# Performance work log

Hardware: AMD Instinct MI355X
Metric: run time of the kernel (lower is better)

## Reference

```python
import jax
import jax.numpy as jnp
from jax import lax
import numpy as np

DIM = 64
HIDDEN = int(DIM * 2.66)      # 170
C2 = HIDDEN * 2               # 340
PATCH = 8


def setup_inputs() -> dict:
    key = jax.random.key(0)
    k1, k2, k3, k4, k5 = jax.random.split(key, 5)
    B, H, W = 4, 256, 256
    x = jax.random.normal(k1, (B, DIM, H, W), dtype=jnp.float32)
    # project_in: 1x1 conv, stored as [out, in]
    w_in = jax.random.normal(k2, (C2, DIM), dtype=jnp.float32) * (1.0 / np.sqrt(DIM))
    # depthwise 3x3 conv weight [C2, 1, 3, 3]
    w_dw = jax.random.normal(k3, (C2, 1, 3, 3), dtype=jnp.float32) * (1.0 / 3.0)
    # learned rFFT filter, init ones in torch; perturb for a nontrivial test
    fft_w = 1.0 + 0.1 * jax.random.normal(k4, (C2, 1, 1, PATCH, PATCH // 2 + 1), dtype=jnp.float32)
    # project_out: 1x1 conv [out, in]
    w_out = jax.random.normal(k5, (DIM, HIDDEN), dtype=jnp.float32) * (1.0 / np.sqrt(HIDDEN))
    return {"x": x, "w_in": w_in, "w_dw": w_dw, "fft_w": fft_w, "w_out": w_out}


def reference(x, w_in, w_dw, fft_w, w_out):
    p = PATCH
    # project_in (1x1 conv)
    x = jnp.einsum('bchw,oc->bohw', x, w_in)
    B, C, H, W = x.shape
    # patchify: b c (h p1) (w p2) -> b c h w p1 p2
    xp = x.reshape(B, C, H // p, p, W // p, p).transpose(0, 1, 2, 4, 3, 5)
    # per-patch rFFT2, elementwise learned filter, inverse
    xf = jnp.fft.rfft2(xp)                       # [B,C,h,w,8,5] complex
    xf = xf * fft_w                              # fft_w broadcasts [C,1,1,8,5]
    xp = jnp.fft.irfft2(xf, s=(p, p))
    # unpatchify
    x = xp.transpose(0, 1, 2, 4, 3, 5).reshape(B, C, H, W)
    # depthwise 3x3 conv, padding 1
    x = lax.conv_general_dilated(
        x, w_dw, window_strides=(1, 1), padding=((1, 1), (1, 1)),
        dimension_numbers=('NCHW', 'OIHW', 'NCHW'), feature_group_count=C)
    # GELU gate
    x1, x2 = jnp.split(x, 2, axis=1)
    x = jax.nn.gelu(x1, approximate=False) * x2
    # project_out (1x1 conv)
    return jnp.einsum('bchw,oc->bohw', x, w_out)
```

## Files before the change

kernel.cpp:

```cpp
#include <hip/hip_runtime.h>
#include <hip/hip_bf16.h>

#define C2 340
#define HID 170
#define NB 4
#define HGT 256
#define WID 256
#define HW (HGT*WID)
#define BAND 128

typedef unsigned short u16;
typedef unsigned int u32;
typedef float f32x4 __attribute__((ext_vector_type(4)));
typedef short s16x8 __attribute__((ext_vector_type(8)));

__device__ __forceinline__ float bf2f(u16 u) {
  union { u32 i; float f; } v; v.i = ((u32)u) << 16; return v.f;
}
__device__ __forceinline__ u16 f2bf(float f) {
  union { float f; u32 i; } v; v.f = f;
  u32 x = v.i;
  return (u16)((x + 0x7fffu + ((x >> 16) & 1u)) >> 16);
}

__device__ __forceinline__ float gelu(float v) {
  const float u = v * 0.70710678118654752f;
  const float ax = fabsf(u);
  const float t = __builtin_amdgcn_rcpf(__builtin_fmaf(0.3275911f, ax, 1.f));
  float p = __builtin_fmaf(1.061405429f, t, -1.453152027f);
  p = __builtin_fmaf(p, t, 1.421413741f);
  p = __builtin_fmaf(p, t, -0.284496736f);
  p = __builtin_fmaf(p, t, 0.254829592f);
  const float e = __builtin_amdgcn_exp2f(-1.4426950408889634f * ax * ax);
  float er = 1.f - p * t * e;
  er = copysignf(er, u);
  return 0.5f * v * (1.f + er);
}

__device__ const float COSTAB[8] = {1.f, 0.70710678118654752f, 0.f, -0.70710678118654752f,
                                    -1.f, -0.70710678118654752f, 0.f, 0.70710678118654752f};

__global__ __launch_bounds__(256) void k_prep(const float* __restrict__ w_in,
                                              const float* __restrict__ w_out,
                                              const float* __restrict__ fw,
                                              u16* __restrict__ wf,
                                              u16* __restrict__ wof,
                                              u16* __restrict__ mf) {
  __shared__ float kern[64];
  const int blk = blockIdx.x;
  if (blk < C2) {
    const int c = blk;
    if (threadIdx.x < 64) {
      const int a = threadIdx.x >> 3, bb = threadIdx.x & 7;
      float acc = 0.f;
      for (int u = 0; u < 8; ++u)
        for (int v = 0; v < 8; ++v) {
          const float wv = (v <= 4) ? fw[c*40 + u*5 + v]
                                    : fw[c*40 + ((8-u)&7)*5 + (8-v)];
          acc += wv * COSTAB[(u*a + v*bb) & 7];
        }
      kern[threadIdx.x] = acc * (1.f/64.f);
    }
    __syncthreads();
    #pragma unroll
    for (int q = 0; q < 16; ++q) {
      const int e = q * 256 + threadIdx.x;
      const int r = e & 7;
      const int l = (e >> 3) & 63;
      const int sb = e >> 9;
      const int s = sb & 1, nblk = sb >> 1;
      const int k = s*32 + ((l >> 4) << 3) + r;
      const int a = k >> 3, bcol = k & 7;
      const int n = nblk*16 + (l & 15);
      const int i = n >> 3, j = n & 7;
      mf[(size_t)c * 4096 + e] = f2bf(kern[(((i - a) & 7) << 3) + ((j - bcol) & 7)]);
    }
  } else if (blk == C2) {
    for (int e = threadIdx.x; e < 22*2*64*8; e += 256) {
      const int r = e & 7;
      const int l = (e >> 3) & 63;
      const int ts = e >> 9;
      const int s = ts & 1, t = ts >> 1;
      const int m = t*16 + (l & 15);
      const int k = s*32 + ((l >> 4) << 3) + r;
      wf[e] = (m < C2) ? f2bf(w_in[m*64 + k]) : (u16)0;
    }
  } else {
    for (int e = threadIdx.x; e < 4*6*64*8; e += 256) {
      const int r = e & 7;
      const int l = (e >> 3) & 63;
      const int mk = e >> 9;
      const int kc = mk % 6, mt = mk / 6;
      const int m = mt*16 + (l & 15);
      const int k = kc*32 + ((l >> 4) << 3) + r;
      wof[e] = (k < HID) ? f2bf(w_out[m*HID + k]) : (u16)0;
    }
  }
}

__global__ __launch_bounds__(256) void k_projin2(const float* __restrict__ x,
                                                 const u16* __restrict__ wf,
                                                 u16* __restrict__ mid) {
  __shared__ __align__(16) u16 st[16][264];
  const int b = blockIdx.x >> 8;
  const int pix_blk = (blockIdx.x & 255) << 8;
  const int w = threadIdx.x >> 6;
  const int lane = threadIdx.x & 63;
  const int lm = lane & 15, lh = lane >> 4;
  const int pix0 = pix_blk + w*64;

  s16x8 Bf[4][2];
  {
    const float* xp = x + (size_t)b * 64 * HW + pix0;
    #pragma unroll
    for (int g = 0; g < 4; ++g)
      #pragma unroll
      for (int s = 0; s < 2; ++s) {
        s16x8 t;
        #pragma unroll
        for (int r = 0; r < 8; ++r) {
          const int ch = s*32 + lh*8 + r;
          t[r] = (short)f2bf(xp[(size_t)ch * HW + g*16 + lm]);
        }
        Bf[g][s] = t;
      }
  }
  u16* mp = mid + (size_t)b * C2 * HW + pix_blk;
  const int ch_rd = threadIdx.x >> 4;
  const int seg = threadIdx.x & 15;
  for (int t = 0; t < 22; ++t) {
    const s16x8 A0 = *(const s16x8*)(wf + ((t*2 + 0)*64 + lane)*8);
    const s16x8 A1 = *(const s16x8*)(wf + ((t*2 + 1)*64 + lane)*8);
    f32x4 ac[4];
    #pragma unroll
    for (int g = 0; g < 4; ++g) {
      ac[g] = (f32x4){0.f,0.f,0.f,0.f};
      ac[g] = __builtin_amdgcn_mfma_f32_16x16x32_bf16(A0, Bf[g][0], ac[g], 0,0,0);
      ac[g] = __builtin_amdgcn_mfma_f32_16x16x32_bf16(A1, Bf[g][1], ac[g], 0,0,0);
    }
    __syncthreads();
    #pragma unroll
    for (int g = 0; g < 4; ++g)
      #pragma unroll
      for (int r = 0; r < 4; ++r)
        st[lh*4 + r][w*64 + g*16 + lm] = f2bf(ac[g][r]);
    __syncthreads();
    const int ch = t*16 + ch_rd;
    if (ch < C2) {
      u16* dst = mp + (size_t)ch * HW + seg*16;
      *(uint4*)dst       = *(const uint4*)&st[ch_rd][seg*16];
      *(uint4*)(dst + 8) = *(const uint4*)&st[ch_rd][seg*16 + 8];
    }
  }
}

__global__ __launch_bounds__(512) void k_pcgate(const u16* __restrict__ mid,
                                                const u16* __restrict__ mf,
                                                const float* __restrict__ w_dw,
                                                u16* __restrict__ gbuf, int hb) {
  __shared__ __align__(16) u16 st[2][18][272];
  const int c = blockIdx.x % HID;
  const int b = blockIdx.x / HID;
  const int P0 = hb >> 3;

  const int w = threadIdx.x >> 6;
  const int lane = threadIdx.x & 63;
  const int lm = lane & 15, lh = lane >> 4;
  const int ch2 = w >> 2;
  const int wl = w & 3;
  const int prow_sub = wl >> 1;
  const int phalf = wl & 1;
  const int ch = c + ch2*HID;
  const int colbase = (phalf*16 + lh*4)*8 + (lm & 7) + 8;

  for (int i = threadIdx.x; i < 2*18*34; i += 512)
    ((uint4*)st)[i] = make_uint4(0,0,0,0);

  s16x8 Bc[4][2];
  const u16* mfc = mf + (size_t)ch * 4096;
  #pragma unroll
  for (int nb = 0; nb < 4; ++nb)
    #pragma unroll
    for (int ks = 0; ks < 2; ++ks)
      Bc[nb][ks] = *(const s16x8*)(mfc + ((nb*2 + ks)*64 + lane)*8);
  const u16* chan = mid + (size_t)(b*C2 + ch) * HW;
  const float* wd1 = w_dw + c * 9;
  const float* wd2 = w_dw + (c + HID) * 9;
  __syncthreads();

  for (int it = 0; it < 8; ++it) {
    const int py2 = P0 + it*2 + 2;
    if (it == 0) {
      for (int i = threadIdx.x; i < 2*34; i += 512)
        ((uint4*)&st[i/34][0][0])[i%34] = make_uint4(0,0,0,0);
    } else {
      for (int i = threadIdx.x; i < 2*34; i += 512)
        ((uint4*)&st[i/34][0][0])[i%34] = ((const uint4*)&st[i/34][16][0])[i%34];
    }
    if (py2 >= 32) {
      for (int i = threadIdx.x; i < 2*34; i += 512)
        ((uint4*)&st[i/34][17][0])[i%34] = make_uint4(0,0,0,0);
    }
    __syncthreads();
    {
      const int py = P0 + it*2 + prow_sub;
      const u16* aptr = chan + (size_t)(py*8 + lh)*WID + (phalf*16 + lm)*8;
      const s16x8 A0 = *(const s16x8*)(aptr);
      const s16x8 A1 = *(const s16x8*)(aptr + 4*WID);
      const int rowb = 1 + prow_sub*8 + (lm >> 3);
      #pragma unroll
      for (int nb = 0; nb < 4; ++nb) {
        f32x4 acc = {0.f,0.f,0.f,0.f};
        acc = __builtin_amdgcn_mfma_f32_16x16x32_bf16(A0, Bc[nb][0], acc, 0,0,0);
        acc = __builtin_amdgcn_mfma_f32_16x16x32_bf16(A1, Bc[nb][1], acc, 0,0,0);
        #pragma unroll
        for (int r = 0; r < 4; ++r)
          st[ch2][rowb + nb*2][colbase + r*8] = f2bf(acc[r]);
      }
    }
    if (wl < 2) {
      if (py2 < 32) {
        const u16* ap = chan + (size_t)(py2*8 + lh)*WID + (phalf*16 + lm)*8;
        const s16x8 A0 = *(const s16x8*)(ap);
        const s16x8 A1 = *(const s16x8*)(ap + 4*WID);
        f32x4 acc = {0.f,0.f,0.f,0.f};
        acc = __builtin_amdgcn_mfma_f32_16x16x32_bf16(A0, Bc[0][0], acc, 0,0,0);
        acc = __builtin_amdgcn_mfma_f32_16x16x32_bf16(A1, Bc[0][1], acc, 0,0,0);
        if ((lm >> 3) == 0) {
          #pragma unroll
          for (int r = 0; r < 4; ++r)
            st[ch2][17][colbase + r*8] = f2bf(acc[r]);
        }
      }
    } else if (it == 0) {
      const int pym = P0 - 1;
      if (pym >= 0) {
        const u16* ap = chan + (size_t)(pym*8 + lh)*WID + (phalf*16 + lm)*8;
        const s16x8 A0 = *(const s16x8*)(ap);
        const s16x8 A1 = *(const s16x8*)(ap + 4*WID);
        f32x4 acc = {0.f,0.f,0.f,0.f};
        acc = __builtin_amdgcn_mfma_f32_16x16x32_bf16(A0, Bc[3][0], acc, 0,0,0);
        acc = __builtin_amdgcn_mfma_f32_16x16x32_bf16(A1, Bc[3][1], acc, 0,0,0);
        if ((lm >> 3) == 1) {
          #pragma unroll
          for (int r = 0; r < 4; ++r)
            st[ch2][0][colbase + r*8] = f2bf(acc[r]);
        }
      }
    }
    __syncthreads();
    {
      const int rg = threadIdx.x >> 5;
      const int px0 = (threadIdx.x & 31) * 8;
      float ax[8], ay[8];
      #pragma unroll
      for (int p = 0; p < 8; ++p) { ax[p] = 0.f; ay[p] = 0.f; }
      #pragma unroll
      for (int wr = 0; wr < 3; ++wr) {
        const u16* r1 = &st[0][rg + wr][px0];
        const u16* r2 = &st[1][rg + wr][px0];
        const s16x8 L1 = *(const s16x8*)r1, M1 = *(const s16x8*)(r1 + 8), R1 = *(const s16x8*)(r1 + 16);
        const s16x8 L2 = *(const s16x8*)r2, M2 = *(const s16x8*)(r2 + 8), R2 = *(const s16x8*)(r2 + 16);
        float cx[10], cy[10];
        cx[0] = bf2f((u16)L1[7]);  cy[0] = bf2f((u16)L2[7]);
        #pragma unroll
        for (int p = 0; p < 8; ++p) { cx[p+1] = bf2f((u16)M1[p]); cy[p+1] = bf2f((u16)M2[p]); }
        cx[9] = bf2f((u16)R1[0]);  cy[9] = bf2f((u16)R2[0]);
        const float w1a = wd1[wr*3+0], w1b = wd1[wr*3+1], w1c = wd1[wr*3+2];
        const float w2a = wd2[wr*3+0], w2b = wd2[wr*3+1], w2c = wd2[wr*3+2];
        #pragma unroll
        for (int p = 0; p < 8; ++p) {
          ax[p] += w1a*cx[p] + w1b*cx[p+1] + w1c*cx[p+2];
          ay[p] += w2a*cy[p] + w2b*cy[p+1] + w2c*cy[p+2];
        }
      }
      u32 pk[4];
      #pragma unroll
      for (int p2 = 0; p2 < 4; ++p2) {
        const float g0 = gelu(ax[2*p2])   * ay[2*p2];
        const float g1 = gelu(ax[2*p2+1]) * ay[2*p2+1];
        pk[p2] = (u32)f2bf(g0) | ((u32)f2bf(g1) << 16);
      }
      u16* gp = gbuf + (((size_t)(b*HID + c)) * BAND + (size_t)(it*16 + rg)) * WID + px0;
      *(uint4*)gp = make_uint4(pk[0], pk[1], pk[2], pk[3]);
    }
    __syncthreads();
  }
}

__global__ __launch_bounds__(256) void k_projout2(const u16* __restrict__ gbuf,
                                                  const u16* __restrict__ wof,
                                                  float* __restrict__ out, int hb) {
  const int b = blockIdx.x >> 7;
  const int p0 = (blockIdx.x & 127) << 8;
  const int w = threadIdx.x >> 6;
  const int lane = threadIdx.x & 63;
  const int lm = lane & 15, lh = lane >> 4;
  const size_t BW = (size_t)BAND * WID;
  const u16* gb = gbuf + (size_t)b * HID * BW + p0 + w*64 + lm;

  f32x4 acc[4][4];
  #pragma unroll
  for (int mt = 0; mt < 4; ++mt)
    #pragma unroll
    for (int ng = 0; ng < 4; ++ng)
      acc[mt][ng] = (f32x4){0.f,0.f,0.f,0.f};

  #pragma unroll
  for (int kc = 0; kc < 6; ++kc) {
    s16x8 A[4];
    #pragma unroll
    for (int mt = 0; mt < 4; ++mt)
      A[mt] = *(const s16x8*)(wof + ((mt*6 + kc)*64 + lane)*8);
    #pragma unroll
    for (int ng = 0; ng < 4; ++ng) {
      s16x8 Bf;
      #pragma unroll
      for (int r = 0; r < 8; ++r) {
        int c = kc*32 + lh*8 + r;
        if (kc == 5) c = min(c, HID - 1);
        Bf[r] = (short)gb[(size_t)c * BW + ng*16];
      }
      #pragma unroll
      for (int mt = 0; mt < 4; ++mt)
        acc[mt][ng] = __builtin_amdgcn_mfma_f32_16x16x32_bf16(A[mt], Bf, acc[mt][ng], 0,0,0);
    }
  }
  float* ob = out + (size_t)b * 64 * HW + (size_t)hb * WID + p0 + w*64 + lm;
  #pragma unroll
  for (int mt = 0; mt < 4; ++mt)
    #pragma unroll
    for (int ng = 0; ng < 4; ++ng)
      #pragma unroll
      for (int r = 0; r < 4; ++r)
        ob[(size_t)(mt*16 + lh*4 + r) * HW + ng*16] = acc[mt][ng][r];
}

extern "C" void kernel_launch(void* const* d_in, const int* in_sizes, int n_in,
                              void* d_out, int out_size, void* d_ws, size_t ws_size,
                              hipStream_t stream) {
  const float* x     = (const float*)d_in[0];
  const float* w_in  = (const float*)d_in[1];
  const float* w_dw  = (const float*)d_in[2];
  const float* fw    = (const float*)d_in[3];
  const float* w_out = (const float*)d_in[4];
  float* out = (float*)d_out;

  char* ws = (char*)d_ws;
  u16* mid    = (u16*)ws;
  u16* gbuf   = (u16*)(ws + 178257920);
  u16* wof    = (u16*)(ws + 178257920 + 44564480);
  u16* mfrag  = (u16*)(ws + 178257920 + 44564480 + 43520);
  u16* wfrag  = (u16*)(ws + 178257920 + 44564480 + 43520 + 2785280);

  k_prep<<<C2 + 2, 256, 0, stream>>>(w_in, w_out, fw, wfrag, wof, mfrag);
  k_projin2<<<NB*256, 256, 0, stream>>>(x, wfrag, mid);
  for (int sb = 0; sb < 2; ++sb) {
    const int hb = sb * BAND;
    k_pcgate<<<NB*HID, 512, 0, stream>>>(mid, mfrag, w_dw, gbuf, hb);
    k_projout2<<<NB*BAND, 256, 0, stream>>>(gbuf, wof, out, hb);
  }
}
```

Measured before the change: 263.4 us.

## Double-buffer depthwise stage tile and recompute halo rows to drop barriers

Switches the k_pcgate shared-memory tile to two alternating buffers. Each iteration now recomputes the top halo row from the previous patch row with an extra MFMA instead of copying it from the prior tile. This removes the halo-copy phase and two of the three __syncthreads per iteration. In exchange it doubles LDS use, which can cut occupancy, and adds redundant MFMA work plus global loads for the halo row.

```diff
diff --git a/kernel.cpp b/kernel.cpp
--- a/kernel.cpp
+++ b/kernel.cpp
@@ -158,7 +158,7 @@
                                                 const u16* __restrict__ mf,
                                                 const float* __restrict__ w_dw,
                                                 u16* __restrict__ gbuf, int hb) {
-  __shared__ __align__(16) u16 st[2][18][272];
+  __shared__ __align__(16) u16 st[2][2][18][272];
   const int c = blockIdx.x % HID;
   const int b = blockIdx.x / HID;
   const int P0 = hb >> 3;
@@ -173,7 +173,7 @@
   const int ch = c + ch2*HID;
   const int colbase = (phalf*16 + lh*4)*8 + (lm & 7) + 8;
 
-  for (int i = threadIdx.x; i < 2*18*34; i += 512)
+  for (int i = threadIdx.x; i < 2*2*18*34; i += 512)
     ((uint4*)st)[i] = make_uint4(0,0,0,0);
 
   s16x8 Bc[4][2];
@@ -189,19 +189,8 @@
   __syncthreads();
 
   for (int it = 0; it < 8; ++it) {
-    const int py2 = P0 + it*2 + 2;
-    if (it == 0) {
-      for (int i = threadIdx.x; i < 2*34; i += 512)
-        ((uint4*)&st[i/34][0][0])[i%34] = make_uint4(0,0,0,0);
-    } else {
-      for (int i = threadIdx.x; i < 2*34; i += 512)
-        ((uint4*)&st[i/34][0][0])[i%34] = ((const uint4*)&st[i/34][16][0])[i%34];
-    }
-    if (py2 >= 32) {
-      for (int i = threadIdx.x; i < 2*34; i += 512)
-        ((uint4*)&st[i/34][17][0])[i%34] = make_uint4(0,0,0,0);
-    }
-    __syncthreads();
+    const int cur = it & 1;
+    u16 (* __restrict__ sb)[18][272] = st[cur];
     {
       const int py = P0 + it*2 + prow_sub;
       const u16* aptr = chan + (size_t)(py*8 + lh)*WID + (phalf*16 + lm)*8;
@@ -215,37 +204,38 @@
         acc = __builtin_amdgcn_mfma_f32_16x16x32_bf16(A1, Bc[nb][1], acc, 0,0,0);
         #pragma unroll
         for (int r = 0; r < 4; ++r)
-          st[ch2][rowb + nb*2][colbase + r*8] = f2bf(acc[r]);
+          sb[ch2][rowb + nb*2][colbase + r*8] = f2bf(acc[r]);
       }
     }
     if (wl < 2) {
+      const int py2 = P0 + it*2 + 2;
+      f32x4 acc = {0.f,0.f,0.f,0.f};
       if (py2 < 32) {
         const u16* ap = chan + (size_t)(py2*8 + lh)*WID + (phalf*16 + lm)*8;
         const s16x8 A0 = *(const s16x8*)(ap);
         const s16x8 A1 = *(const s16x8*)(ap + 4*WID);
-        f32x4 acc = {0.f,0.f,0.f,0.f};
         acc = __builtin_amdgcn_mfma_f32_16x16x32_bf16(A0, Bc[0][0], acc, 0,0,0);
         acc = __builtin_amdgcn_mfma_f32_16x16x32_bf16(A1, Bc[0][1], acc, 0,0,0);
-        if ((lm >> 3) == 0) {
-          #pragma unroll
-          for (int r = 0; r < 4; ++r)
-            st[ch2][17][colbase + r*8] = f2bf(acc[r]);
-        }
-      }
-    } else if (it == 0) {
-      const int pym = P0 - 1;
+      }
+      if ((lm >> 3) == 0) {
+        #pragma unroll
+        for (int r = 0; r < 4; ++r)
+          sb[ch2][17][colbase + r*8] = f2bf(acc[r]);
+      }
+    } else {
+      const int pym = P0 + it*2 - 1;
+      f32x4 acc = {0.f,0.f,0.f,0.f};
       if (pym >= 0) {
         const u16* ap = chan + (size_t)(pym*8 + lh)*WID + (phalf*16 + lm)*8;
         const s16x8 A0 = *(const s16x8*)(ap);
         const s16x8 A1 = *(const s16x8*)(ap + 4*WID);
-        f32x4 acc = {0.f,0.f,0.f,0.f};
         acc = __builtin_amdgcn_mfma_f32_16x16x32_bf16(A0, Bc[3][0], acc, 0,0,0);
         acc = __builtin_amdgcn_mfma_f32_16x16x32_bf16(A1, Bc[3][1], acc, 0,0,0);
-        if ((lm >> 3) == 1) {
-          #pragma unroll
-          for (int r = 0; r < 4; ++r)
-            st[ch2][0][colbase + r*8] = f2bf(acc[r]);
-        }
+      }
+      if ((lm >> 3) == 1) {
+        #pragma unroll
+        for (int r = 0; r < 4; ++r)
+          sb[ch2][0][colbase + r*8] = f2bf(acc[r]);
       }
     }
     __syncthreads();
@@ -257,8 +247,8 @@
       for (int p = 0; p < 8; ++p) { ax[p] = 0.f; ay[p] = 0.f; }
       #pragma unroll
       for (int wr = 0; wr < 3; ++wr) {
-        const u16* r1 = &st[0][rg + wr][px0];
-        const u16* r2 = &st[1][rg + wr][px0];
+        const u16* r1 = &sb[0][rg + wr][px0];
+        const u16* r2 = &sb[1][rg + wr][px0];
         const s16x8 L1 = *(const s16x8*)r1, M1 = *(const s16x8*)(r1 + 8), R1 = *(const s16x8*)(r1 + 16);
         const s16x8 L2 = *(const s16x8*)r2, M2 = *(const s16x8*)(r2 + 8), R2 = *(const s16x8*)(r2 + 16);
         float cx[10], cy[10];
@@ -284,7 +274,6 @@
       u16* gp = gbuf + (((size_t)(b*HID + c)) * BAND + (size_t)(it*16 + rg)) * WID + px0;
       *(uint4*)gp = make_uint4(pk[0], pk[1], pk[2], pk[3]);
     }
-    __syncthreads();
   }
 }
 
```

New measurement: 227.3 us (median of 2 runs). 13.7% less time.
